# Performance work log

Hardware: AMD Instinct MI355X
Metric: run time of the kernel (lower is better)

Reference implementation:

```python
import jax, jax.numpy as jnp
import numpy as np

# Mixed-precision group-quantized attention (MicroMix QLlamaAttention reference).
P4, P6, P8 = 2048, 1024, 1024   # 4/6/8-bit column partitions of in_features=4096
NUM_HEADS = 32
HEAD_DIM = 128
ROPE_THETA = 10000.0
GROUP = 32                       # scale-factor group size (from SFB* sizing: out*p//32)


def _fake_quant(x, bits):
    # symmetric per-32-element-group quantize->dequantize along last axis
    maxq = 2.0 ** (bits - 1) - 1.0
    g = x.reshape(x.shape[:-1] + (-1, GROUP))
    s = jnp.max(jnp.abs(g), axis=-1, keepdims=True) / maxq
    s = jnp.where(s == 0, jnp.ones_like(s), s)
    dq = (jnp.clip(jnp.round(g / s), -maxq - 1.0, maxq) * s).reshape(x.shape)
    return dq


def _mixed_quant(x):
    # reorder_index is identity in this module; columns are partitioned [p4|p6|p8]
    xn = _fake_quant(x[..., :P4], 4)
    xs = _fake_quant(x[..., P4:P4 + P6], 6)
    xo = _fake_quant(x[..., P4 + P6:], 8)
    return jnp.concatenate([xn, xs, xo], axis=-1)


def _qlinear(x, W):
    # mixedgemm.matmul: dequantized activation @ dequantized weight^T (W is [out,in])
    return jnp.einsum('...k,nk->...n', _mixed_quant(x), _mixed_quant(W))


def _rope(x):
    # LLaMA rotary embedding (rotate-half), fused into attention in flashinfer
    b, s, h, d = x.shape
    inv = 1.0 / (ROPE_THETA ** (jnp.arange(0, d, 2, dtype=jnp.float32) / d))
    ang = jnp.arange(s, dtype=jnp.float32)[:, None] * inv[None, :]  # [s, d/2]
    cos = jnp.cos(ang)[None, :, None, :]
    sin = jnp.sin(ang)[None, :, None, :]
    x1, x2 = x[..., : d // 2], x[..., d // 2:]
    return jnp.concatenate([x1 * cos - x2 * sin, x2 * cos + x1 * sin], axis=-1)


def setup_inputs() -> dict:
    key = jax.random.key(0)
    k0, k1, k2, k3, k4 = jax.random.split(key, 5)
    H = 4096
    inp = {
        'hidden_states': jax.random.normal(k0, (2, 1024, H), dtype=jnp.float32),
        'Wq': jax.random.normal(k1, (H, H), dtype=jnp.float32) * 0.02,
        'Wk': jax.random.normal(k2, (H, H), dtype=jnp.float32) * 0.02,
        'Wv': jax.random.normal(k3, (H, H), dtype=jnp.float32) * 0.02,
        'Wo': jax.random.normal(k4, (H, H), dtype=jnp.float32) * 0.02,
    }
    return inp


def reference(hidden_states, Wq, Wk, Wv, Wo):
    b, s, h = hidden_states.shape
    q = _qlinear(hidden_states, Wq).reshape(b, s, NUM_HEADS, HEAD_DIM)
    k = _qlinear(hidden_states, Wk).reshape(b, s, NUM_HEADS, HEAD_DIM)
    v = _qlinear(hidden_states, Wv).reshape(b, s, NUM_HEADS, HEAD_DIM)
    # single_prefill_with_kv_cache(..., causal=True, pos_encoding_mode='ROPE_LLAMA')
    q = _rope(q)
    k = _rope(k)
    scale = 1.0 / np.sqrt(HEAD_DIM)
    scores = jnp.einsum('bqhd,bkhd->bhqk', q, k) * scale
    causal = jnp.tril(jnp.ones((s, s), dtype=bool))
    scores = jnp.where(causal[None, None], scores, jnp.finfo(scores.dtype).min)
    attn = jax.nn.softmax(scores, axis=-1)
    o = jnp.einsum('bhqk,bkhd->bqhd', attn, v).reshape(b * s, h)
    # reorder_quantize_x + o_proj mixed GEMM
    out = _qlinear(o, Wo).reshape(b, s, h)
    return out
```

## Files before the change

### kernel.cpp

```cpp
#include <hip/hip_runtime.h>


typedef __attribute__((ext_vector_type(8))) short bfrag;
typedef __attribute__((ext_vector_type(4))) float ffrag;

#define MFMA16(a, b, c) __builtin_amdgcn_mfma_f32_16x16x32_bf16(a, b, c, 0, 0, 0)

typedef const __attribute__((address_space(1))) unsigned int* gp_t;
typedef __attribute__((address_space(3))) unsigned int* lp_t;

__device__ __forceinline__ unsigned short f2bf(float f) {
  unsigned int u = __float_as_uint(f);
  u += 0x7fffu + ((u >> 16) & 1u);
  return (unsigned short)(u >> 16);
}
__device__ __forceinline__ float bf2f(unsigned short h) {
  return __uint_as_float(((unsigned int)h) << 16);
}

__global__ __launch_bounds__(256) void quant_int_k(
    const float* __restrict__ src, unsigned short* __restrict__ dq,
    float* __restrict__ sT, int ngroups, int nrows) {
  int g = blockIdx.x * 256 + threadIdx.x;
  if (g >= ngroups) return;
  int gc = g & 127;
  int row = g >> 7;
  float maxq = (gc < 64) ? 7.f : ((gc < 96) ? 31.f : 127.f);
  const float4* p = (const float4*)(src + (size_t)g * 32);
  float4 v[8];
  float amax = 0.f;
#pragma unroll
  for (int i = 0; i < 8; ++i) {
    v[i] = p[i];
    amax = fmaxf(amax, fmaxf(fmaxf(fabsf(v[i].x), fabsf(v[i].y)),
                             fmaxf(fabsf(v[i].z), fabsf(v[i].w))));
  }
  float s = amax / maxq;
  if (s == 0.f) s = 1.f;
  float lc = -maxq - 1.f;
  ushort4* qo = (ushort4*)(dq + (size_t)g * 32);
#pragma unroll
  for (int i = 0; i < 8; ++i) {
    float xs[4] = {v[i].x, v[i].y, v[i].z, v[i].w};
    ushort4 hh;
    unsigned short* hp = (unsigned short*)&hh;
#pragma unroll
    for (int j = 0; j < 4; ++j) {
      float q = rintf(xs[j] / s);
      q = fminf(fmaxf(q, lc), maxq);
      hp[j] = f2bf(q);
    }
    qo[i] = hh;
  }
  sT[(size_t)gc * nrows + row] = s;
}

__global__ __launch_bounds__(256) void rope_split_k(
    const float* __restrict__ src, unsigned short* __restrict__ hi,
    unsigned short* __restrict__ lo) {
  int idx = blockIdx.x * 256 + threadIdx.x;
  int dp = idx & 63;
  int h = (idx >> 6) & 31;
  int tok = idx >> 11;
  int si = tok & 1023;
  size_t base = (size_t)tok * 4096 + h * 128 + dp;
  float x1 = src[base];
  float x2 = src[base + 64];
  float inv = powf(10000.f, -(float)dp * (1.f / 64.f));
  float ang = (float)si * inv;
  float sn, cs;
  sincosf(ang, &sn, &cs);
  float o1 = x1 * cs - x2 * sn;
  float o2 = x2 * cs + x1 * sn;
  unsigned short h1 = f2bf(o1), h2 = f2bf(o2);
  hi[base] = h1;
  lo[base] = f2bf(o1 - bf2f(h1));
  hi[base + 64] = h2;
  lo[base + 64] = f2bf(o2 - bf2f(h2));
}

__global__ __launch_bounds__(256, 2) void gemm_int_k(
    const unsigned short* __restrict__ Aq, const float* __restrict__ AsT,
    const unsigned short* __restrict__ Bq, const float* __restrict__ BsT,
    float* __restrict__ Cf, unsigned short* __restrict__ Chi,
    unsigned short* __restrict__ Clo, int M, int N, int K, int mode) {
  __shared__ unsigned short sA[2][128 * 64];
  __shared__ unsigned short sB[2][128 * 64];
  __shared__ float sSA[2][256], sSB[2][256];
  int tid = threadIdx.x;
  int w = tid >> 6, lane = tid & 63, quad = lane >> 4, c = lane & 15;
  int wm = w >> 1, wn = w & 1;
  int bm = blockIdx.y * 128, bn = blockIdx.x * 128;
  int l8 = lane >> 3, l7 = lane & 7;
  int sp = tid >> 7, sidx = tid & 127;
  ffrag acc[4][4] = {};
  const ffrag fz = {};

  auto STAGE = [&](int buf, int k0) {
    int g = k0 >> 5;
    __builtin_amdgcn_global_load_lds(
        (gp_t)(AsT + (size_t)(g + sp) * M + bm + sidx),
        (lp_t)&sSA[buf][w * 64], 4, 0, 0);
    __builtin_amdgcn_global_load_lds(
        (gp_t)(BsT + (size_t)(g + sp) * N + bn + sidx),
        (lp_t)&sSB[buf][w * 64], 4, 0, 0);
#pragma unroll
    for (int rr = 0; rr < 4; ++rr) {
      int row = rr * 32 + w * 8 + l8;
      const unsigned short* gA =
          Aq + (size_t)(bm + row) * K + k0 + ((l7 ^ (row & 7)) * 8);
      const unsigned short* gB =
          Bq + (size_t)(bn + row) * K + k0 + ((l7 ^ (row & 7)) * 8);
      __builtin_amdgcn_global_load_lds((gp_t)gA,
                                       (lp_t)&sA[buf][(rr * 32 + w * 8) * 64],
                                       16, 0, 0);
      __builtin_amdgcn_global_load_lds((gp_t)gB,
                                       (lp_t)&sB[buf][(rr * 32 + w * 8) * 64],
                                       16, 0, 0);
    }
  };

  STAGE(0, 0);
  int nt = K >> 6;
  for (int t = 0; t < nt; ++t) {
    int cur = t & 1;
    __syncthreads();
    if (t + 1 < nt) STAGE(cur ^ 1, (t + 1) << 6);
#pragma unroll
    for (int gg2 = 0; gg2 < 2; ++gg2) {
      bfrag av[4], bv[4];
#pragma unroll
      for (int i = 0; i < 4; ++i) {
        int ra = wm * 64 + i * 16 + c;
        int rb = wn * 64 + i * 16 + c;
        av[i] = *(const bfrag*)&sA[cur][ra * 64 + (((gg2 * 4 + quad) ^ (ra & 7)) * 8)];
        bv[i] = *(const bfrag*)&sB[cur][rb * 64 + (((gg2 * 4 + quad) ^ (rb & 7)) * 8)];
      }
      ffrag sx[4];
      float sw4[4];
#pragma unroll
      for (int i = 0; i < 4; ++i)
        sx[i] = *(const ffrag*)&sSA[cur][gg2 * 128 + wm * 64 + i * 16 + quad * 4];
#pragma unroll
      for (int j = 0; j < 4; ++j)
        sw4[j] = sSB[cur][gg2 * 128 + wn * 64 + j * 16 + c];
#pragma unroll
      for (int i = 0; i < 4; ++i)
#pragma unroll
        for (int j = 0; j < 4; ++j) {
          ffrag dot = MFMA16(av[i], bv[j], fz);
          acc[i][j] += dot * (sx[i] * sw4[j]);
        }
    }
  }
#pragma unroll
  for (int i = 0; i < 4; ++i)
#pragma unroll
    for (int j = 0; j < 4; ++j) {
      int m0 = bm + wm * 64 + i * 16 + quad * 4;
      int n = bn + wn * 64 + j * 16 + c;
#pragma unroll
      for (int r = 0; r < 4; ++r) {
        float val = acc[i][j][r];
        if (mode == 1) {
          int tok = m0 + r;
          int bb = tok >> 10, si = tok & 1023;
          int hh = n >> 7, d = n & 127;
          size_t o = ((size_t)(bb * 32 + hh) * 128 + d) * 1024 + si;
          unsigned short hv = f2bf(val);
          Chi[o] = hv;
          Clo[o] = f2bf(val - bf2f(hv));
        } else {
          Cf[(size_t)(m0 + r) * N + n] = val;
        }
      }
    }
}

__global__ __launch_bounds__(256, 2) void attn_k(
    const unsigned short* __restrict__ Qh, const unsigned short* __restrict__ Ql,
    const unsigned short* __restrict__ Khg, const unsigned short* __restrict__ Klg,
    const unsigned short* __restrict__ Vhg, const unsigned short* __restrict__ Vlg,
    float* __restrict__ O) {
  __shared__ unsigned short sKh[2][64 * 128], sKl[2][64 * 128];
  int qb = blockIdx.y, bh = blockIdx.x;
  int b = bh >> 5, h = bh & 31;
  int tid = threadIdx.x;
  int lane = tid & 63, w = tid >> 6, quad = lane >> 4, c = lane & 15;
  int q0 = qb * 64 + w * 16;
  bfrag bqh[4], bql[4];
  {
    const unsigned short* qr = Qh + ((size_t)(b * 1024 + q0 + c)) * 4096 + h * 128 + quad * 8;
    const unsigned short* qrl = Ql + ((size_t)(b * 1024 + q0 + c)) * 4096 + h * 128 + quad * 8;
#pragma unroll
    for (int kd = 0; kd < 4; ++kd) {
      bqh[kd] = *(const bfrag*)(qr + kd * 32);
      bql[kd] = *(const bfrag*)(qrl + kd * 32);
    }
  }
  ffrag oacc[8] = {};
  float m_q = -INFINITY, l_q = 0.f;
  const float scale = 0.088388347648318447f;
  const unsigned short* Kb = Khg + ((size_t)b * 1024) * 4096 + h * 128;
  const unsigned short* Klb = Klg + ((size_t)b * 1024) * 4096 + h * 128;
  const unsigned short* Vb = Vhg + ((size_t)bh * 128) * 1024;
  const unsigned short* Vlb = Vlg + ((size_t)bh * 128) * 1024;
  int sA_ = ((quad & 1) << 5) + c;
  int sB_ = sA_ + 16;
  int sr = lane >> 4, sch = lane & 15;

  auto STAGEK = [&](int buf, int kt) {
#pragma unroll
    for (int rr = 0; rr < 4; ++rr) {
      int row = rr * 16 + w * 4 + sr;
      size_t g = (size_t)(kt * 64 + row) * 4096 + ((sch ^ (row & 15)) * 8);
      __builtin_amdgcn_global_load_lds((gp_t)(Kb + g),
                                       (lp_t)&sKh[buf][(rr * 16 + w * 4) * 128],
                                       16, 0, 0);
      __builtin_amdgcn_global_load_lds((gp_t)(Klb + g),
                                       (lp_t)&sKl[buf][(rr * 16 + w * 4) * 128],
                                       16, 0, 0);
    }
  };

  STAGEK(0, 0);
  for (int kt = 0; kt <= qb; ++kt) {
    int cur = kt & 1;
    __syncthreads();
    if (kt < qb) STAGEK(cur ^ 1, kt + 1);
    ffrag sf[4] = {};
#pragma unroll
    for (int kd = 0; kd < 4; ++kd) {
      bfrag ah[4], al[4];
#pragma unroll
      for (int kb = 0; kb < 4; ++kb) {
        int off = ((kb * 16 + c) * 16 + ((kd * 4 + quad) ^ c)) * 8;
        ah[kb] = *(const bfrag*)&sKh[cur][off];
        al[kb] = *(const bfrag*)&sKl[cur][off];
      }
#pragma unroll
      for (int kb = 0; kb < 4; ++kb) {
        sf[kb] = MFMA16(ah[kb], bqh[kd], sf[kb]);
        sf[kb] = MFMA16(ah[kb], bql[kd], sf[kb]);
        sf[kb] = MFMA16(al[kb], bqh[kd], sf[kb]);
      }
    }
    float rmax = -INFINITY;
    bool diag = (kt == qb);
#pragma unroll
    for (int kb = 0; kb < 4; ++kb)
#pragma unroll
      for (int r = 0; r < 4; ++r) {
        float v = sf[kb][r] * scale;
        if (diag && (kb * 16 + quad * 4 + r) > (w * 16 + c)) v = -1e30f;
        sf[kb][r] = v;
        rmax = fmaxf(rmax, v);
      }
    rmax = fmaxf(rmax, __shfl_xor(rmax, 16, 64));
    rmax = fmaxf(rmax, __shfl_xor(rmax, 32, 64));
    float mn = fmaxf(m_q, rmax);
    float alpha = __expf(m_q - mn);
    m_q = mn;
    bfrag ph[2], pl[2];
    float rsum = 0.f;
#pragma unroll
    for (int sblk = 0; sblk < 2; ++sblk)
#pragma unroll
      for (int j = 0; j < 8; ++j) {
        int srclane = (j < 4) ? sA_ : sB_;
        float v0 = __shfl(sf[sblk * 2 + 0][j & 3], srclane, 64);
        float v1 = __shfl(sf[sblk * 2 + 1][j & 3], srclane, 64);
        float v = (quad < 2) ? v0 : v1;
        float p = __expf(v - m_q);
        rsum += p;
        unsigned short hp = f2bf(p);
        ph[sblk][j] = (short)hp;
        pl[sblk][j] = (short)f2bf(p - bf2f(hp));
      }
    rsum += __shfl_xor(rsum, 16, 64);
    rsum += __shfl_xor(rsum, 32, 64);
    l_q = l_q * alpha + rsum;
    float al4[4];
#pragma unroll
    for (int r = 0; r < 4; ++r) al4[r] = __shfl(alpha, quad * 4 + r, 64);
#pragma unroll
    for (int db = 0; db < 8; ++db)
#pragma unroll
      for (int r = 0; r < 4; ++r) oacc[db][r] *= al4[r];
#pragma unroll
    for (int db = 0; db < 8; ++db) {
      const unsigned short* vrow = Vb + (size_t)(db * 16 + c) * 1024 + kt * 64;
      const unsigned short* vrowl = Vlb + (size_t)(db * 16 + c) * 1024 + kt * 64;
#pragma unroll
      for (int sblk = 0; sblk < 2; ++sblk) {
        bfrag vh_ = *(const bfrag*)(vrow + (sblk * 4 + quad) * 8);
        bfrag vl_ = *(const bfrag*)(vrowl + (sblk * 4 + quad) * 8);
        oacc[db] = MFMA16(ph[sblk], vh_, oacc[db]);
        oacc[db] = MFMA16(ph[sblk], vl_, oacc[db]);
        oacc[db] = MFMA16(pl[sblk], vh_, oacc[db]);
      }
    }
  }
  float invl[4];
#pragma unroll
  for (int r = 0; r < 4; ++r) invl[r] = 1.f / __shfl(l_q, quad * 4 + r, 64);
#pragma unroll
  for (int db = 0; db < 8; ++db)
#pragma unroll
    for (int r = 0; r < 4; ++r)
      O[((size_t)(b * 1024 + q0 + quad * 4 + r)) * 4096 + h * 128 + db * 16 + c] =
          oacc[db][r] * invl[r];
}

extern "C" void kernel_launch(void* const* d_in, const int* in_sizes, int n_in,
                              void* d_out, int out_size, void* d_ws, size_t ws_size,
                              hipStream_t stream) {
  (void)in_sizes; (void)n_in; (void)out_size; (void)ws_size;
  const float* x = (const float*)d_in[0];
  const float* Wq = (const float*)d_in[1];
  const float* Wk = (const float*)d_in[2];
  const float* Wv = (const float*)d_in[3];
  const float* Wo = (const float*)d_in[4];
  float* out = (float*)d_out;
  char* ws = (char*)d_ws;
  const size_t MB = 1024ull * 1024ull;
  unsigned short* Xq = (unsigned short*)(ws);
  float* Xs = (float*)(ws + 16 * MB);
  unsigned short* Wqq = (unsigned short*)(ws + 24 * MB);
  float* Ws = (float*)(ws + 56 * MB);
  float* S1 = (float*)(ws + 64 * MB);
  unsigned short* Qh = (unsigned short*)(ws + 96 * MB);
  unsigned short* Ql = (unsigned short*)(ws + 112 * MB);
  unsigned short* Kh = (unsigned short*)(ws + 128 * MB);
  unsigned short* Kl = (unsigned short*)(ws + 144 * MB);
  unsigned short* Vh = (unsigned short*)(ws + 160 * MB);
  unsigned short* Vl = (unsigned short*)(ws + 176 * MB);

  dim3 gg(32, 16), gb(256);
  quant_int_k<<<1024, 256, 0, stream>>>(x, Xq, Xs, 2048 * 128, 2048);
  quant_int_k<<<2048, 256, 0, stream>>>(Wq, Wqq, Ws, 4096 * 128, 4096);
  gemm_int_k<<<gg, gb, 0, stream>>>(Xq, Xs, Wqq, Ws, S1, nullptr, nullptr,
                                    2048, 4096, 4096, 0);
  rope_split_k<<<16384, 256, 0, stream>>>(S1, Qh, Ql);
  quant_int_k<<<2048, 256, 0, stream>>>(Wk, Wqq, Ws, 4096 * 128, 4096);
  gemm_int_k<<<gg, gb, 0, stream>>>(Xq, Xs, Wqq, Ws, S1, nullptr, nullptr,
                                    2048, 4096, 4096, 0);
  rope_split_k<<<16384, 256, 0, stream>>>(S1, Kh, Kl);
  quant_int_k<<<2048, 256, 0, stream>>>(Wv, Wqq, Ws, 4096 * 128, 4096);
  gemm_int_k<<<gg, gb, 0, stream>>>(Xq, Xs, Wqq, Ws, nullptr, Vh, Vl,
                                    2048, 4096, 4096, 1);
  attn_k<<<dim3(64, 16), 256, 0, stream>>>(Qh, Ql, Kh, Kl, Vh, Vl, S1);
  quant_int_k<<<1024, 256, 0, stream>>>(S1, Xq, Xs, 2048 * 128, 2048);
  quant_int_k<<<2048, 256, 0, stream>>>(Wo, Wqq, Ws, 4096 * 128, 4096);
  gemm_int_k<<<gg, gb, 0, stream>>>(Xq, Xs, Wqq, Ws, out, nullptr, nullptr,
                                    2048, 4096, 4096, 0);
}
```

Measured before the change: 1.104 ms.

## Use 8-wave GEMM blocks, add MFMA priority hints, lazily rescale softmax

The GEMM block grows from 4 to 8 waves (512 threads). Each wave now owns a 64x32 tile instead of 64x64, which cuts per-wave registers and allows more resident waves to hide latency. s_setprio is raised around the MFMA sections in both the GEMM and attention kernels so matrix work is favoured over other waves. The attention kernel also skips the running-max update and accumulator rescale unless some row's max exceeds the stored max by more than 8. This trades an exact running max for fewer exp and multiply operations, and risks larger unnormalised values in exchange.

```diff
diff --git a/kernel.cpp b/kernel.cpp
--- a/kernel.cpp
+++ b/kernel.cpp
@@ -79,7 +79,7 @@
   lo[base + 64] = f2bf(o2 - bf2f(h2));
 }
 
-__global__ __launch_bounds__(256, 2) void gemm_int_k(
+__global__ __launch_bounds__(512, 4) void gemm_int_k(
     const unsigned short* __restrict__ Aq, const float* __restrict__ AsT,
     const unsigned short* __restrict__ Bq, const float* __restrict__ BsT,
     float* __restrict__ Cf, unsigned short* __restrict__ Chi,
@@ -89,33 +89,34 @@
   __shared__ float sSA[2][256], sSB[2][256];
   int tid = threadIdx.x;
   int w = tid >> 6, lane = tid & 63, quad = lane >> 4, c = lane & 15;
-  int wm = w >> 1, wn = w & 1;
+  int wm = w >> 2, wn = w & 3;
   int bm = blockIdx.y * 128, bn = blockIdx.x * 128;
   int l8 = lane >> 3, l7 = lane & 7;
-  int sp = tid >> 7, sidx = tid & 127;
-  ffrag acc[4][4] = {};
+  ffrag acc[4][2] = {};
   const ffrag fz = {};
 
   auto STAGE = [&](int buf, int k0) {
     int g = k0 >> 5;
-    __builtin_amdgcn_global_load_lds(
-        (gp_t)(AsT + (size_t)(g + sp) * M + bm + sidx),
-        (lp_t)&sSA[buf][w * 64], 4, 0, 0);
-    __builtin_amdgcn_global_load_lds(
-        (gp_t)(BsT + (size_t)(g + sp) * N + bn + sidx),
-        (lp_t)&sSB[buf][w * 64], 4, 0, 0);
-#pragma unroll
-    for (int rr = 0; rr < 4; ++rr) {
-      int row = rr * 32 + w * 8 + l8;
+    {
+      int w2 = w & 3;
+      const float* sp = (w < 4)
+          ? (AsT + (size_t)(g + (w2 >> 1)) * M + bm + (w2 & 1) * 64 + lane)
+          : (BsT + (size_t)(g + (w2 >> 1)) * N + bn + (w2 & 1) * 64 + lane);
+      lp_t dst = (w < 4) ? (lp_t)&sSA[buf][w2 * 64] : (lp_t)&sSB[buf][w2 * 64];
+      __builtin_amdgcn_global_load_lds((gp_t)sp, dst, 4, 0, 0);
+    }
+#pragma unroll
+    for (int rr = 0; rr < 2; ++rr) {
+      int row = rr * 64 + w * 8 + l8;
       const unsigned short* gA =
           Aq + (size_t)(bm + row) * K + k0 + ((l7 ^ (row & 7)) * 8);
       const unsigned short* gB =
           Bq + (size_t)(bn + row) * K + k0 + ((l7 ^ (row & 7)) * 8);
       __builtin_amdgcn_global_load_lds((gp_t)gA,
-                                       (lp_t)&sA[buf][(rr * 32 + w * 8) * 64],
+                                       (lp_t)&sA[buf][(rr * 64 + w * 8) * 64],
                                        16, 0, 0);
       __builtin_amdgcn_global_load_lds((gp_t)gB,
-                                       (lp_t)&sB[buf][(rr * 32 + w * 8) * 64],
+                                       (lp_t)&sB[buf][(rr * 64 + w * 8) * 64],
                                        16, 0, 0);
     }
   };
@@ -128,37 +129,42 @@
     if (t + 1 < nt) STAGE(cur ^ 1, (t + 1) << 6);
 #pragma unroll
     for (int gg2 = 0; gg2 < 2; ++gg2) {
-      bfrag av[4], bv[4];
+      bfrag av[4], bv[2];
 #pragma unroll
       for (int i = 0; i < 4; ++i) {
         int ra = wm * 64 + i * 16 + c;
-        int rb = wn * 64 + i * 16 + c;
         av[i] = *(const bfrag*)&sA[cur][ra * 64 + (((gg2 * 4 + quad) ^ (ra & 7)) * 8)];
-        bv[i] = *(const bfrag*)&sB[cur][rb * 64 + (((gg2 * 4 + quad) ^ (rb & 7)) * 8)];
+      }
+#pragma unroll
+      for (int j = 0; j < 2; ++j) {
+        int rb = wn * 32 + j * 16 + c;
+        bv[j] = *(const bfrag*)&sB[cur][rb * 64 + (((gg2 * 4 + quad) ^ (rb & 7)) * 8)];
       }
       ffrag sx[4];
-      float sw4[4];
+      float sw4[2];
 #pragma unroll
       for (int i = 0; i < 4; ++i)
         sx[i] = *(const ffrag*)&sSA[cur][gg2 * 128 + wm * 64 + i * 16 + quad * 4];
 #pragma unroll
-      for (int j = 0; j < 4; ++j)
-        sw4[j] = sSB[cur][gg2 * 128 + wn * 64 + j * 16 + c];
+      for (int j = 0; j < 2; ++j)
+        sw4[j] = sSB[cur][gg2 * 128 + wn * 32 + j * 16 + c];
+      __builtin_amdgcn_s_setprio(1);
 #pragma unroll
       for (int i = 0; i < 4; ++i)
 #pragma unroll
-        for (int j = 0; j < 4; ++j) {
+        for (int j = 0; j < 2; ++j) {
           ffrag dot = MFMA16(av[i], bv[j], fz);
           acc[i][j] += dot * (sx[i] * sw4[j]);
         }
+      __builtin_amdgcn_s_setprio(0);
     }
   }
 #pragma unroll
   for (int i = 0; i < 4; ++i)
 #pragma unroll
-    for (int j = 0; j < 4; ++j) {
+    for (int j = 0; j < 2; ++j) {
       int m0 = bm + wm * 64 + i * 16 + quad * 4;
-      int n = bn + wn * 64 + j * 16 + c;
+      int n = bn + wn * 32 + j * 16 + c;
 #pragma unroll
       for (int r = 0; r < 4; ++r) {
         float val = acc[i][j][r];
@@ -229,6 +235,7 @@
     __syncthreads();
     if (kt < qb) STAGEK(cur ^ 1, kt + 1);
     ffrag sf[4] = {};
+    __builtin_amdgcn_s_setprio(1);
 #pragma unroll
     for (int kd = 0; kd < 4; ++kd) {
       bfrag ah[4], al[4];
@@ -245,6 +252,7 @@
         sf[kb] = MFMA16(al[kb], bqh[kd], sf[kb]);
       }
     }
+    __builtin_amdgcn_s_setprio(0);
     float rmax = -INFINITY;
     bool diag = (kt == qb);
 #pragma unroll
@@ -258,9 +266,19 @@
       }
     rmax = fmaxf(rmax, __shfl_xor(rmax, 16, 64));
     rmax = fmaxf(rmax, __shfl_xor(rmax, 32, 64));
-    float mn = fmaxf(m_q, rmax);
-    float alpha = __expf(m_q - mn);
-    m_q = mn;
+    if (!__all(rmax <= m_q + 8.f)) {
+      float mn = fmaxf(m_q, rmax);
+      float alpha = __expf(m_q - mn);
+      m_q = mn;
+      l_q *= alpha;
+      float al4[4];
+#pragma unroll
+      for (int r = 0; r < 4; ++r) al4[r] = __shfl(alpha, quad * 4 + r, 64);
+#pragma unroll
+      for (int db = 0; db < 8; ++db)
+#pragma unroll
+        for (int r = 0; r < 4; ++r) oacc[db][r] *= al4[r];
+    }
     bfrag ph[2], pl[2];
     float rsum = 0.f;
 #pragma unroll
@@ -279,14 +297,8 @@
       }
     rsum += __shfl_xor(rsum, 16, 64);
     rsum += __shfl_xor(rsum, 32, 64);
-    l_q = l_q * alpha + rsum;
-    float al4[4];
-#pragma unroll
-    for (int r = 0; r < 4; ++r) al4[r] = __shfl(alpha, quad * 4 + r, 64);
-#pragma unroll
-    for (int db = 0; db < 8; ++db)
-#pragma unroll
-      for (int r = 0; r < 4; ++r) oacc[db][r] *= al4[r];
+    l_q += rsum;
+    __builtin_amdgcn_s_setprio(1);
 #pragma unroll
     for (int db = 0; db < 8; ++db) {
       const unsigned short* vrow = Vb + (size_t)(db * 16 + c) * 1024 + kt * 64;
@@ -300,6 +312,7 @@
         oacc[db] = MFMA16(pl[sblk], vh_, oacc[db]);
       }
     }
+    __builtin_amdgcn_s_setprio(0);
   }
   float invl[4];
 #pragma unroll
@@ -336,22 +349,22 @@
   unsigned short* Vh = (unsigned short*)(ws + 160 * MB);
   unsigned short* Vl = (unsigned short*)(ws + 176 * MB);
 
-  dim3 gg(32, 16), gb(256);
+  dim3 gg(32, 16);
   quant_int_k<<<1024, 256, 0, stream>>>(x, Xq, Xs, 2048 * 128, 2048);
   quant_int_k<<<2048, 256, 0, stream>>>(Wq, Wqq, Ws, 4096 * 128, 4096);
-  gemm_int_k<<<gg, gb, 0, stream>>>(Xq, Xs, Wqq, Ws, S1, nullptr, nullptr,
-                                    2048, 4096, 4096, 0);
+  gemm_int_k<<<gg, 512, 0, stream>>>(Xq, Xs, Wqq, Ws, S1, nullptr, nullptr,
+                                     2048, 4096, 4096, 0);
   rope_split_k<<<16384, 256, 0, stream>>>(S1, Qh, Ql);
   quant_int_k<<<2048, 256, 0, stream>>>(Wk, Wqq, Ws, 4096 * 128, 4096);
-  gemm_int_k<<<gg, gb, 0, stream>>>(Xq, Xs, Wqq, Ws, S1, nullptr, nullptr,
-                                    2048, 4096, 4096, 0);
+  gemm_int_k<<<gg, 512, 0, stream>>>(Xq, Xs, Wqq, Ws, S1, nullptr, nullptr,
+                                     2048, 4096, 4096, 0);
   rope_split_k<<<16384, 256, 0, stream>>>(S1, Kh, Kl);
   quant_int_k<<<2048, 256, 0, stream>>>(Wv, Wqq, Ws, 4096 * 128, 4096);
-  gemm_int_k<<<gg, gb, 0, stream>>>(Xq, Xs, Wqq, Ws, nullptr, Vh, Vl,
-                                    2048, 4096, 4096, 1);
+  gemm_int_k<<<gg, 512, 0, stream>>>(Xq, Xs, Wqq, Ws, nullptr, Vh, Vl,
+                                     2048, 4096, 4096, 1);
   attn_k<<<dim3(64, 16), 256, 0, stream>>>(Qh, Ql, Kh, Kl, Vh, Vl, S1);
   quant_int_k<<<1024, 256, 0, stream>>>(S1, Xq, Xs, 2048 * 128, 2048);
   quant_int_k<<<2048, 256, 0, stream>>>(Wo, Wqq, Ws, 4096 * 128, 4096);
-  gemm_int_k<<<gg, gb, 0, stream>>>(Xq, Xs, Wqq, Ws, out, nullptr, nullptr,
-                                    2048, 4096, 4096, 0);
-}
+  gemm_int_k<<<gg, 512, 0, stream>>>(Xq, Xs, Wqq, Ws, out, nullptr, nullptr,
+                                     2048, 4096, 4096, 0);
+}
```

Result: faster. 1.023 ms (-7.3%).
